# Kernel tuning notes

Measured on AMD Instinct MI355X. Metric: run time of the kernel, lower is better.

## Reference

```python
import jax, jax.numpy as jnp
import numpy as np

N_NODES = 100000
N_EDGES = 3200000
N_FEAT = 128
N_GRAPHS = 512


def setup_inputs() -> dict:
    key = jax.random.key(0)
    ks = jax.random.split(key, 12)
    x = jax.random.normal(ks[0], (N_NODES, N_FEAT), dtype=jnp.float32)
    edge_index = jax.random.randint(ks[1], (2, N_EDGES), 0, N_NODES, dtype=jnp.int64)
    batch = jnp.sort(jax.random.randint(ks[2], (N_NODES,), 0, N_GRAPHS, dtype=jnp.int64))
    def glorot(k, shape):
        lim = float(np.sqrt(6.0 / (shape[0] + shape[1])))
        return jax.random.uniform(k, shape, jnp.float32, -lim, lim)
    return {
        "x": x,
        "edge_index": edge_index,
        "batch": batch,
        "W1": glorot(ks[3], (N_FEAT, 32)),
        "b1": jnp.zeros((32,), jnp.float32),
        "W2": glorot(ks[4], (32, 64)),
        "b2": jnp.zeros((64,), jnp.float32),
        "fW1": glorot(ks[5], (96, 128)),
        "fb1": jnp.zeros((128,), jnp.float32),
        "fW2": glorot(ks[6], (128, 1)),
        "fb2": jnp.zeros((1,), jnp.float32),
    }


def _gcn_conv(h, W, b, src, dst, norm, n):
    # linear transform then normalized scatter-add aggregation (PyG GCNConv)
    h = h @ W                               # [N, out]
    msg = h[src] * norm[:, None]            # gather + scale, [E+N, out]
    agg = jax.ops.segment_sum(msg, dst, num_segments=n)
    return agg + b


def reference(x, edge_index, batch, W1, b1, W2, b2, fW1, fb1, fW2, fb2):
    n = x.shape[0]
    loop = jnp.arange(n, dtype=edge_index.dtype)
    src = jnp.concatenate([edge_index[0], loop])  # add self-loops
    dst = jnp.concatenate([edge_index[1], loop])
    # symmetric normalization: D^{-1/2} A_hat D^{-1/2}
    deg = jax.ops.segment_sum(jnp.ones(src.shape, x.dtype), dst, num_segments=n)
    dinv = jnp.where(deg > 0, jax.lax.rsqrt(deg), 0.0)
    norm = dinv[src] * dinv[dst]

    x1 = jax.nn.relu(_gcn_conv(x, W1, b1, src, dst, norm, n))   # [N, 32]
    x2 = jax.nn.relu(_gcn_conv(x1, W2, b2, src, dst, norm, n))  # [N, 64]
    xj = jnp.concatenate([x1, x2], axis=-1)                      # JK 'cat' -> [N, 96]

    # global_mean_pool over graphs
    sums = jax.ops.segment_sum(xj, batch, num_segments=N_GRAPHS)
    cnt = jax.ops.segment_sum(jnp.ones((n,), x.dtype), batch, num_segments=N_GRAPHS)
    pooled = sums / jnp.maximum(cnt, 1.0)[:, None]               # [G, 96]

    h = jax.nn.relu(pooled @ fW1 + fb1)
    return (h @ fW2 + fb2).reshape(-1)                           # [G]
```

## Files before the change

kernel.cpp:

```cpp
#include <hip/hip_runtime.h>
#include <stdint.h>

#define FEAT_IN 128
#define F1 32
#define F2 64
#define FJ 96
#define FH 128

#define BSH 8
#define BNODES 256
#define NBMAX 512
#define CH 4096
#define SRCBITS 17
#define SRCMASK 0x1FFFFu
#define PADMAX 768
#define PNPB 256
#define NP2 64
#define GR 64
#define XPAD 132

__device__ __forceinline__ unsigned f2bf(float f) {
    unsigned u = __float_as_uint(f);
    return (u + 0x7FFFu + ((u >> 16) & 1u)) >> 16;
}
__device__ __forceinline__ float bf2f(unsigned h) { return __uint_as_float(h << 16); }
__device__ __forceinline__ void bfacc8(float* a, uint4 v) {
    a[0] += bf2f(v.x & 0xffffu); a[1] += bf2f(v.x >> 16);
    a[2] += bf2f(v.y & 0xffffu); a[3] += bf2f(v.y >> 16);
    a[4] += bf2f(v.z & 0xffffu); a[5] += bf2f(v.z >> 16);
    a[6] += bf2f(v.w & 0xffffu); a[7] += bf2f(v.w >> 16);
}
__device__ __forceinline__ void fma4(float* acc, float s, float4 wv) {
    acc[0] = fmaf(s, wv.x, acc[0]);
    acc[1] = fmaf(s, wv.y, acc[1]);
    acc[2] = fmaf(s, wv.z, acc[2]);
    acc[3] = fmaf(s, wv.w, acc[3]);
}

__global__ void histPB(const int* __restrict__ dst, int* __restrict__ gHistT,
                       int nE, int nB, int nChP) {
    __shared__ int h[NBMAX];
    int ck = blockIdx.x, t = threadIdx.x;
    int e0 = ck * CH;
    int ecnt = min(CH, nE - e0);
    if (ecnt <= 0) return;
    for (int i = t; i < nB; i += 256) h[i] = 0;
    __syncthreads();
    for (int i = t; i < ecnt; i += 256) atomicAdd(&h[dst[e0 + i] >> BSH], 1);
    __syncthreads();
    for (int b = t; b < nB; b += 256) gHistT[(size_t)b * nChP + ck] = h[b];
}

__global__ void __launch_bounds__(256)
scanWB(const int* __restrict__ gHistT, int* __restrict__ gBaseT,
       int* __restrict__ btot, int nB, int nChP) {
    int wv = blockIdx.x * 4 + (threadIdx.x >> 6);
    if (wv >= nB) return;
    int lane = threadIdx.x & 63;
    const int* hp = gHistT + (size_t)wv * nChP;
    int* gp = gBaseT + (size_t)wv * nChP;
    int running = 0;
    for (int c0 = 0; c0 < nChP; c0 += 64) {
        int ck = c0 + lane;
        int v = (ck < nChP) ? hp[ck] : 0;
        int incl = v;
#pragma unroll
        for (int off = 1; off < 64; off <<= 1) {
            int u = __shfl_up(incl, off);
            if (lane >= off) incl += u;
        }
        if (ck < nChP) gp[ck] = running + incl - v;
        running += __shfl(incl, 63);
    }
    if (lane == 0) btot[wv] = running;
}

__global__ void __launch_bounds__(512)
scanOff(const int* __restrict__ btot, int* __restrict__ boff, int nB) {
    __shared__ int ps[512];
    int t = threadIdx.x;
    int v = (t < nB) ? btot[t] : 0;
    ps[t] = v; __syncthreads();
    for (int off = 1; off < 512; off <<= 1) {
        int u = (t >= off) ? ps[t - off] : 0; __syncthreads();
        ps[t] += u; __syncthreads();
    }
    int excl = ps[t] - v;
    if (t < nB) boff[t] = excl;
    if (t == nB - 1) boff[nB] = excl + v;
}

__global__ void __launch_bounds__(256)
scatterEB2(const int* __restrict__ src, const int* __restrict__ dst,
           const int* __restrict__ gBaseT, const int* __restrict__ boff,
           unsigned* __restrict__ EB, int nE, int nB, int nChP) {
    __shared__ int lh[NBMAX], loff[NBMAX], lcur[NBMAX], gbaseL[NBMAX];
    __shared__ int ps[256];
    __shared__ unsigned stagePack[CH];
    __shared__ unsigned short stageBkt[CH];
    int ck = blockIdx.x, t = threadIdx.x;
    int e0 = ck * CH;
    int ecnt = min(CH, nE - e0);
    if (ecnt <= 0) return;
    for (int i = t; i < nB; i += 256) lh[i] = 0;
    __syncthreads();
    for (int i = t; i < ecnt; i += 256) atomicAdd(&lh[dst[e0 + i] >> BSH], 1);
    __syncthreads();
    int b0 = 2 * t, b1 = 2 * t + 1;
    int c0 = (b0 < nB) ? lh[b0] : 0;
    int c1 = (b1 < nB) ? lh[b1] : 0;
    ps[t] = c0 + c1; __syncthreads();
    for (int off = 1; off < 256; off <<= 1) {
        int v = (t >= off) ? ps[t - off] : 0; __syncthreads();
        ps[t] += v; __syncthreads();
    }
    int excl = ps[t] - (c0 + c1);
    if (b0 < nB) { loff[b0] = excl;      lcur[b0] = excl;      gbaseL[b0] = boff[b0] + gBaseT[(size_t)b0 * nChP + ck]; }
    if (b1 < nB) { loff[b1] = excl + c0; lcur[b1] = excl + c0; gbaseL[b1] = boff[b1] + gBaseT[(size_t)b1 * nChP + ck]; }
    __syncthreads();
    for (int i = t; i < ecnt; i += 256) {
        int d = dst[e0 + i], s = src[e0 + i];
        int bkt = d >> BSH;
        int p = atomicAdd(&lcur[bkt], 1);
        stagePack[p] = (unsigned)s | ((unsigned)(d & (BNODES - 1)) << SRCBITS);
        stageBkt[p] = (unsigned short)bkt;
    }
    __syncthreads();
    for (int i = t; i < ecnt; i += 256) {
        int bb = stageBkt[i];
        EB[gbaseL[bb] + (i - loff[bb])] = stagePack[i];
    }
}

__global__ void __launch_bounds__(512)
bucketSortK(const unsigned* __restrict__ EB, const int* __restrict__ boff,
            int* __restrict__ rowptr, int* __restrict__ rowend, int* __restrict__ csrP,
            float* __restrict__ dinv, float* __restrict__ rs, int nN, int nB) {
    __shared__ int hist[BNODES];
    __shared__ int cur[BNODES];
    __shared__ int ps[256];
    int b = blockIdx.x, t = threadIdx.x;
    int beg = boff[b], end = boff[b + 1];
    if (t < 256) hist[t] = 0;
    __syncthreads();
    for (int i = beg + t; i < end; i += 512) atomicAdd(&hist[EB[i] >> SRCBITS], 1);
    __syncthreads();
    int deg = (t < 256) ? hist[t] : 0;
    int pdeg = (deg + 3) & ~3;
    if (t < 256) ps[t] = pdeg;
    __syncthreads();
    for (int off = 1; off < 256; off <<= 1) {
        int v = (t >= off && t < 256) ? ps[t - off] : 0; __syncthreads();
        if (t < 256) ps[t] += v;
        __syncthreads();
    }
    int base = ((beg + 3) & ~3) + b * PADMAX;
    int excl = 0;
    if (t < 256) {
        excl = base + ps[t] - pdeg;
        int node = (b << BSH) + t;
        if (node < nN) {
            rowptr[node] = excl;
            rowend[node] = excl + pdeg;
            dinv[node] = rsqrtf((float)deg + 1.0f);
            rs[node] = sqrtf((float)deg + 1.0f);
        }
        cur[t] = excl;
    }
    __syncthreads();
    for (int i = beg + t; i < end; i += 512) {
        unsigned v = EB[i];
        int p = atomicAdd(&cur[v >> SRCBITS], 1);
        csrP[p] = (int)(v & SRCMASK);
    }
    __syncthreads();
    if (t < 256) {
        for (int p = cur[t]; p < excl + pdeg; ++p) csrP[p] = nN;
    }
}

__global__ void __launch_bounds__(256)
gemm1v3(const float4* __restrict__ x4, const float* __restrict__ W1,
        const float* __restrict__ dinv, unsigned* __restrict__ Gc, int nN) {
    __shared__ float Ws[FEAT_IN * F1];
    __shared__ float xs[GR * XPAD];
    int t = threadIdx.x;
    for (int i = t; i < FEAT_IN * F1; i += 256) Ws[i] = W1[i];
    int rb = blockIdx.x * GR;
    for (int i = t; i < GR * 32; i += 256) {
        int r = i >> 5, c = i & 31;
        int row = rb + r;
        float4 v = (row < nN) ? x4[(size_t)row * 32 + c] : make_float4(0.f, 0.f, 0.f, 0.f);
        *(float4*)(xs + r * XPAD + c * 4) = v;
    }
    __syncthreads();
    int cg = t & 7, rg = t >> 3;
    int r0 = rg * 2, r1 = r0 + 1;
    int j0 = cg * 4;
    float acc0[4] = {0.f, 0.f, 0.f, 0.f};
    float acc1[4] = {0.f, 0.f, 0.f, 0.f};
    const float4* xa4 = (const float4*)(xs + r0 * XPAD);
    const float4* xb4 = (const float4*)(xs + r1 * XPAD);
    const float4* W4 = (const float4*)Ws;
#pragma unroll 4
    for (int kc = 0; kc < 32; ++kc) {
        float4 xa = xa4[kc];
        float4 xb = xb4[kc];
        float4 w0 = W4[(4 * kc + 0) * 8 + cg];
        float4 w1 = W4[(4 * kc + 1) * 8 + cg];
        float4 w2 = W4[(4 * kc + 2) * 8 + cg];
        float4 w3 = W4[(4 * kc + 3) * 8 + cg];
        fma4(acc0, xa.x, w0); fma4(acc0, xa.y, w1);
        fma4(acc0, xa.z, w2); fma4(acc0, xa.w, w3);
        fma4(acc1, xb.x, w0); fma4(acc1, xb.y, w1);
        fma4(acc1, xb.z, w2); fma4(acc1, xb.w, w3);
    }
    int c = j0 >> 4;
    int w = (j0 & 15) >> 1;
    int row0 = rb + r0, row1 = rb + r1;
    if (row0 < nN) {
        float dv = dinv[row0];
        uint2 val;
        val.x = f2bf(acc0[0] * dv) | (f2bf(acc0[1] * dv) << 16);
        val.y = f2bf(acc0[2] * dv) | (f2bf(acc0[3] * dv) << 16);
        *(uint2*)(Gc + ((size_t)c * (nN + 1) + row0) * 8 + w) = val;
    }
    if (row1 < nN) {
        float dv = dinv[row1];
        uint2 val;
        val.x = f2bf(acc1[0] * dv) | (f2bf(acc1[1] * dv) << 16);
        val.y = f2bf(acc1[2] * dv) | (f2bf(acc1[3] * dv) << 16);
        *(uint2*)(Gc + ((size_t)c * (nN + 1) + row1) * 8 + w) = val;
    }
}

__global__ void __launch_bounds__(256)
agg1v2(const int* __restrict__ rowptr, const int* __restrict__ rowend,
       const int* __restrict__ csrP, const unsigned* __restrict__ Gc,
       const float* __restrict__ dinv, const float* __restrict__ b1,
       unsigned* __restrict__ Hc, int nN, int K) {
    int b = blockIdx.x;
    int xcd = b & 7;
    int c = xcd & 1;
    int k = (b >> 3) * 4 + (xcd >> 1);
    if (k >= K) return;
    int t = threadIdx.x, wv = t >> 6, lane = t & 63;
    int node = k * 16 + wv * 4 + (lane >> 4);
    int slot = (lane >> 1) & 7, comp = lane & 1;
    bool vn = node < nN;
    const uint4* Gch = (const uint4*)(Gc + (size_t)c * (nN + 1) * 8);
    float a[8] = {0, 0, 0, 0, 0, 0, 0, 0};
    if (vn) {
        if ((lane & 14) == 0) bfacc8(a, Gch[(size_t)node * 2 + comp]);
        int beg = rowptr[node], endp = rowend[node];
        for (int e = beg + slot * 4; e < endp; e += 32) {
            int4 idx = *(const int4*)(csrP + e);
            uint4 r0 = Gch[(size_t)idx.x * 2 + comp];
            uint4 r1 = Gch[(size_t)idx.y * 2 + comp];
            uint4 r2 = Gch[(size_t)idx.z * 2 + comp];
            uint4 r3 = Gch[(size_t)idx.w * 2 + comp];
            bfacc8(a, r0); bfacc8(a, r1); bfacc8(a, r2); bfacc8(a, r3);
        }
    }
#pragma unroll
    for (int m = 2; m < 16; m <<= 1) {
#pragma unroll
        for (int i = 0; i < 8; ++i) a[i] += __shfl_xor(a[i], m);
    }
    if (vn && (lane & 14) == 0) {
        float dv = dinv[node];
        const float* bb = b1 + c * 16 + comp * 8;
        float h[8];
#pragma unroll
        for (int i = 0; i < 8; ++i) {
            float x1 = fmaxf(fmaf(dv, a[i], bb[i]), 0.f);
            h[i] = dv * x1;
        }
        uint4 hp;
        hp.x = f2bf(h[0]) | (f2bf(h[1]) << 16);
        hp.y = f2bf(h[2]) | (f2bf(h[3]) << 16);
        hp.z = f2bf(h[4]) | (f2bf(h[5]) << 16);
        hp.w = f2bf(h[6]) | (f2bf(h[7]) << 16);
        ((uint4*)(Hc + (size_t)c * (nN + 1) * 8))[(size_t)node * 2 + comp] = hp;
    }
}

__global__ void __launch_bounds__(256)
agg2v2(const int* __restrict__ rowptr, const int* __restrict__ rowend,
       const int* __restrict__ csrP, const unsigned* __restrict__ Hc,
       const float* __restrict__ dinv, float* __restrict__ A2, int nN, int K) {
    int b = blockIdx.x;
    int xcd = b & 7;
    int c = xcd & 1;
    int k = (b >> 3) * 4 + (xcd >> 1);
    if (k >= K) return;
    int t = threadIdx.x, wv = t >> 6, lane = t & 63;
    int node = k * 16 + wv * 4 + (lane >> 4);
    int slot = (lane >> 1) & 7, comp = lane & 1;
    bool vn = node < nN;
    const uint4* Hch = (const uint4*)(Hc + (size_t)c * (nN + 1) * 8);
    float a[8] = {0, 0, 0, 0, 0, 0, 0, 0};
    if (vn) {
        if ((lane & 14) == 0) bfacc8(a, Hch[(size_t)node * 2 + comp]);
        int beg = rowptr[node], endp = rowend[node];
        for (int e = beg + slot * 4; e < endp; e += 32) {
            int4 idx = *(const int4*)(csrP + e);
            uint4 r0 = Hch[(size_t)idx.x * 2 + comp];
            uint4 r1 = Hch[(size_t)idx.y * 2 + comp];
            uint4 r2 = Hch[(size_t)idx.z * 2 + comp];
            uint4 r3 = Hch[(size_t)idx.w * 2 + comp];
            bfacc8(a, r0); bfacc8(a, r1); bfacc8(a, r2); bfacc8(a, r3);
        }
    }
#pragma unroll
    for (int m = 2; m < 16; m <<= 1) {
#pragma unroll
        for (int i = 0; i < 8; ++i) a[i] += __shfl_xor(a[i], m);
    }
    if (vn && (lane & 14) == 0) {
        float dv = dinv[node];
        float* dst = A2 + (size_t)node * F1 + c * 16 + comp * 8;
        float4 o0 = make_float4(dv * a[0], dv * a[1], dv * a[2], dv * a[3]);
        float4 o1 = make_float4(dv * a[4], dv * a[5], dv * a[6], dv * a[7]);
        ((float4*)dst)[0] = o0;
        ((float4*)dst)[1] = o1;
    }
}

__global__ void __launch_bounds__(256)
poolX1(const unsigned* __restrict__ Hc, const float* __restrict__ rs,
       const int* __restrict__ batch, float* __restrict__ psum, int nN) {
    int t = threadIdx.x, wv = t >> 6, lane = t & 63;
    int c = wv >> 1, half = wv & 1;
    int base = blockIdx.x * PNPB + half * (PNPB / 2);
    int w32 = lane & 7, noff = lane >> 3;
    const unsigned* Hch = Hc + (size_t)c * (nN + 1) * 8;
    int feat = c * 16 + w32 * 2;
    float a0 = 0.f, a1 = 0.f;
    int curG = -1;
#pragma unroll 4
    for (int i = 0; i < PNPB / 16; ++i) {
        int node = base + noff + 8 * i;
        if (node >= nN) break;
        int bg = batch[node];
        if (bg != curG) {
            if (curG >= 0) {
                atomicAdd(&psum[(size_t)curG * FJ + feat + 0], a0);
                atomicAdd(&psum[(size_t)curG * FJ + feat + 1], a1);
            }
            a0 = a1 = 0.f; curG = bg;
        }
        unsigned v = Hch[(size_t)node * 8 + w32];
        float r = rs[node];
        a0 = fmaf(bf2f(v & 0xffffu), r, a0);
        a1 = fmaf(bf2f(v >> 16), r, a1);
    }
    if (curG >= 0) {
        atomicAdd(&psum[(size_t)curG * FJ + feat + 0], a0);
        atomicAdd(&psum[(size_t)curG * FJ + feat + 1], a1);
    }
}

__global__ void __launch_bounds__(256)
poolX2(const float* __restrict__ A2, const float* __restrict__ W2,
       const float* __restrict__ b2, const int* __restrict__ batch,
       float* __restrict__ psum, int nN) {
    __shared__ float W2s[F1 * F2];
    __shared__ float aL[NP2][F1];
    int t = threadIdx.x;
    for (int i = t; i < F1 * F2; i += 256) W2s[i] = W2[i];
    int nbase = blockIdx.x * NP2;
    {
        const float4* A4 = (const float4*)(A2 + (size_t)nbase * F1);
        float4* aL4 = (float4*)aL;
        int total4 = NP2 * F1 / 4;
        for (int i = t; i < total4; i += 256) {
            int gnode = nbase + (i >> 3);
            aL4[i] = (gnode < nN) ? A4[i] : make_float4(0.f, 0.f, 0.f, 0.f);
        }
    }
    __syncthreads();
    int wv = t >> 6, lane = t & 63;
    int n0 = wv * (NP2 / 4);
    float bj = b2[lane];
    float acc = 0.f;
    int curG = -1;
    for (int i = 0; i < NP2 / 4; ++i) {
        int node = nbase + n0 + i;
        if (node >= nN) break;
        int bg = batch[node];
        if (bg != curG) {
            if (curG >= 0) atomicAdd(&psum[(size_t)curG * FJ + F1 + lane], acc);
            acc = 0.f; curG = bg;
        }
        const float* a = aL[n0 + i];
        float dot = 0.f;
#pragma unroll
        for (int k = 0; k < F1; ++k) dot = fmaf(a[k], W2s[k * F2 + lane], dot);
        acc += fmaxf(dot + bj, 0.f);
    }
    if (curG >= 0) atomicAdd(&psum[(size_t)curG * FJ + F1 + lane], acc);
}

__global__ void cntBS(const int* __restrict__ batch, float* __restrict__ cnt,
                      int nN, int nG) {
    int g = blockIdx.x * blockDim.x + threadIdx.x;
    if (g >= nG) return;
    int lo = 0, hi = nN;
    while (lo < hi) { int m = (lo + hi) >> 1; if (batch[m] < g) lo = m + 1; else hi = m; }
    int s = lo;
    lo = 0; hi = nN;
    while (lo < hi) { int m = (lo + hi) >> 1; if (batch[m] < g + 1) lo = m + 1; else hi = m; }
    cnt[g] = (float)(lo - s);
}

__global__ void mlp_kernel(const float* __restrict__ psum, const float* __restrict__ cnt,
                           const float* __restrict__ fW1, const float* __restrict__ fb1,
                           const float* __restrict__ fW2, const float* __restrict__ fb2,
                           float* __restrict__ out) {
    __shared__ float p[FJ];
    __shared__ float red[FH];
    int g = blockIdx.x, tid = threadIdx.x;
    float c = fmaxf(cnt[g], 1.0f);
    if (tid < FJ) p[tid] = psum[g * FJ + tid] / c;
    __syncthreads();
    float acc = fb1[tid];
    for (int k = 0; k < FJ; ++k) acc = fmaf(p[k], fW1[k * FH + tid], acc);
    float h = fmaxf(acc, 0.f);
    red[tid] = h * fW2[tid];
    __syncthreads();
    for (int s = FH / 2; s > 0; s >>= 1) {
        if (tid < s) red[tid] += red[tid + s];
        __syncthreads();
    }
    if (tid == 0) out[g] = red[0] + fb2[0];
}

extern "C" void kernel_launch(void* const* d_in, const int* in_sizes, int n_in,
                              void* d_out, int out_size, void* d_ws, size_t ws_size,
                              hipStream_t stream) {
    const float* x   = (const float*)d_in[0];
    const int*   ei  = (const int*)d_in[1];
    const int*   bat = (const int*)d_in[2];
    const float* W1  = (const float*)d_in[3];
    const float* b1  = (const float*)d_in[4];
    const float* W2  = (const float*)d_in[5];
    const float* b2  = (const float*)d_in[6];
    const float* fW1 = (const float*)d_in[7];
    const float* fb1 = (const float*)d_in[8];
    const float* fW2 = (const float*)d_in[9];
    const float* fb2 = (const float*)d_in[10];
    float* out = (float*)d_out;

    int nN = in_sizes[0] / FEAT_IN;
    int nE = in_sizes[1] / 2;
    int nG = out_size;
    const int* src = ei;
    const int* dst = ei + nE;

    int nB   = (nN + BNODES - 1) >> BSH;
    int nCh  = (nE + CH - 1) / CH;
    int nChP = (nCh + 3) & ~3;
    int K    = (nN + 15) / 16;
    int gridC = ((K + 3) / 4) * 8;

    char* w = (char*)d_ws;
    auto alloc = [&](size_t bytes) { char* p = w; w += (bytes + 15) & ~(size_t)15; return p; };
    int*      gHistT = (int*)alloc((size_t)NBMAX * nChP * 4);
    int*      gBaseT = (int*)alloc((size_t)NBMAX * nChP * 4);
    int*      btot   = (int*)alloc(NBMAX * 4);
    int*      boff   = (int*)alloc((NBMAX + 1) * 4);
    unsigned* EB     = (unsigned*)alloc((size_t)nE * 4);
    int*      rowptr = (int*)alloc((size_t)nN * 4);
    int*      rowend = (int*)alloc((size_t)nN * 4);
    int*      csrP   = (int*)alloc(((size_t)nE + (size_t)NBMAX * PADMAX + 64) * 4);
    float*    dinv   = (float*)alloc((size_t)nN * 4);
    float*    rsb    = (float*)alloc((size_t)nN * 4);
    unsigned* Gc     = (unsigned*)alloc((size_t)2 * (nN + 1) * 16 * 2);
    unsigned* Hc     = (unsigned*)alloc((size_t)2 * (nN + 1) * 16 * 2);
    float*    A2     = (float*)alloc((size_t)(nN + NP2) * F1 * 4);
    float*    psum   = (float*)alloc((size_t)nG * FJ * 4);
    float*    cnt    = (float*)alloc((size_t)nG * 4);

    hipMemsetAsync(gHistT, 0, (size_t)nB * nChP * 4, stream);
    hipMemsetAsync(psum, 0, (size_t)nG * FJ * 4, stream);
    for (int c = 0; c < 2; ++c) {
        hipMemsetAsync(Gc + ((size_t)c * (nN + 1) + nN) * 16, 0, 32, stream);
        hipMemsetAsync(Hc + ((size_t)c * (nN + 1) + nN) * 16, 0, 32, stream);
    }

    histPB<<<nCh, 256, 0, stream>>>(dst, gHistT, nE, nB, nChP);
    scanWB<<<(nB + 3) / 4, 256, 0, stream>>>(gHistT, gBaseT, btot, nB, nChP);
    scanOff<<<1, 512, 0, stream>>>(btot, boff, nB);
    scatterEB2<<<nCh, 256, 0, stream>>>(src, dst, gBaseT, boff, EB, nE, nB, nChP);
    bucketSortK<<<nB, 512, 0, stream>>>(EB, boff, rowptr, rowend, csrP, dinv, rsb, nN, nB);

    gemm1v3<<<(nN + GR - 1) / GR, 256, 0, stream>>>((const float4*)x, W1, dinv, Gc, nN);
    agg1v2<<<gridC, 256, 0, stream>>>(rowptr, rowend, csrP, Gc, dinv, b1, Hc, nN, K);
    agg2v2<<<gridC, 256, 0, stream>>>(rowptr, rowend, csrP, Hc, dinv, A2, nN, K);

    poolX1<<<(nN + PNPB - 1) / PNPB, 256, 0, stream>>>(Hc, rsb, bat, psum, nN);
    poolX2<<<(nN + NP2 - 1) / NP2, 256, 0, stream>>>(A2, W2, b2, bat, psum, nN);
    cntBS<<<(nG + 255) / 256, 256, 0, stream>>>(bat, cnt, nN, nG);
    mlp_kernel<<<nG, FH, 0, stream>>>(psum, cnt, fW1, fb1, fW2, fb2, out);
}
```

Before: 254.3 us.

## Store layer-2 aggregate in bf16, fold memsets and count kernel into others

Several independent tweaks. The layer-2 aggregate A2 is now written as packed bf16 instead of fp32, halving that intermediate's traffic, and poolX2 unpacks it into shared memory. The four small pad-row memsets are replaced by writes inside gemm1v3, and the separate cntBS kernel is folded into mlp_kernel via a per-block binary search. The histogram layout becomes chunk-major, so histPB writes contiguously while scanWB reads strided, and bf16 unpacking of the high half uses a mask instead of a shift. The bf16 storage adds rounding error to the layer-2 input before the W2 transform.

```diff
diff --git a/kernel.cpp b/kernel.cpp
--- a/kernel.cpp
+++ b/kernel.cpp
@@ -23,12 +23,13 @@
     unsigned u = __float_as_uint(f);
     return (u + 0x7FFFu + ((u >> 16) & 1u)) >> 16;
 }
-__device__ __forceinline__ float bf2f(unsigned h) { return __uint_as_float(h << 16); }
+__device__ __forceinline__ float bf2f_lo(unsigned u) { return __uint_as_float(u << 16); }
+__device__ __forceinline__ float bf2f_hi(unsigned u) { return __uint_as_float(u & 0xffff0000u); }
 __device__ __forceinline__ void bfacc8(float* a, uint4 v) {
-    a[0] += bf2f(v.x & 0xffffu); a[1] += bf2f(v.x >> 16);
-    a[2] += bf2f(v.y & 0xffffu); a[3] += bf2f(v.y >> 16);
-    a[4] += bf2f(v.z & 0xffffu); a[5] += bf2f(v.z >> 16);
-    a[6] += bf2f(v.w & 0xffffu); a[7] += bf2f(v.w >> 16);
+    a[0] += bf2f_lo(v.x); a[1] += bf2f_hi(v.x);
+    a[2] += bf2f_lo(v.y); a[3] += bf2f_hi(v.y);
+    a[4] += bf2f_lo(v.z); a[5] += bf2f_hi(v.z);
+    a[6] += bf2f_lo(v.w); a[7] += bf2f_hi(v.w);
 }
 __device__ __forceinline__ void fma4(float* acc, float s, float4 wv) {
     acc[0] = fmaf(s, wv.x, acc[0]);
@@ -37,8 +38,8 @@
     acc[3] = fmaf(s, wv.w, acc[3]);
 }
 
-__global__ void histPB(const int* __restrict__ dst, int* __restrict__ gHistT,
-                       int nE, int nB, int nChP) {
+__global__ void histPB(const int* __restrict__ dst, int* __restrict__ gHist,
+                       int nE, int nB) {
     __shared__ int h[NBMAX];
     int ck = blockIdx.x, t = threadIdx.x;
     int e0 = ck * CH;
@@ -48,21 +49,20 @@
     __syncthreads();
     for (int i = t; i < ecnt; i += 256) atomicAdd(&h[dst[e0 + i] >> BSH], 1);
     __syncthreads();
-    for (int b = t; b < nB; b += 256) gHistT[(size_t)b * nChP + ck] = h[b];
-}
-
-__global__ void __launch_bounds__(256)
-scanWB(const int* __restrict__ gHistT, int* __restrict__ gBaseT,
+    for (int b = t; b < nB; b += 256) gHist[(size_t)ck * NBMAX + b] = h[b];
+}
+
+__global__ void __launch_bounds__(256)
+scanWB(const int* __restrict__ gHist, int* __restrict__ gBaseT,
        int* __restrict__ btot, int nB, int nChP) {
     int wv = blockIdx.x * 4 + (threadIdx.x >> 6);
     if (wv >= nB) return;
     int lane = threadIdx.x & 63;
-    const int* hp = gHistT + (size_t)wv * nChP;
     int* gp = gBaseT + (size_t)wv * nChP;
     int running = 0;
     for (int c0 = 0; c0 < nChP; c0 += 64) {
         int ck = c0 + lane;
-        int v = (ck < nChP) ? hp[ck] : 0;
+        int v = (ck < nChP) ? gHist[(size_t)ck * NBMAX + wv] : 0;
         int incl = v;
 #pragma unroll
         for (int off = 1; off < 64; off <<= 1) {
@@ -181,10 +181,15 @@
 
 __global__ void __launch_bounds__(256)
 gemm1v3(const float4* __restrict__ x4, const float* __restrict__ W1,
-        const float* __restrict__ dinv, unsigned* __restrict__ Gc, int nN) {
+        const float* __restrict__ dinv, unsigned* __restrict__ Gc,
+        unsigned* __restrict__ Hc, int nN) {
     __shared__ float Ws[FEAT_IN * F1];
     __shared__ float xs[GR * XPAD];
     int t = threadIdx.x;
+    if (blockIdx.x == 0 && t < 16) {
+        Gc[((size_t)(t >> 3) * (nN + 1) + nN) * 8 + (t & 7)] = 0u;
+        Hc[((size_t)(t >> 3) * (nN + 1) + nN) * 8 + (t & 7)] = 0u;
+    }
     for (int i = t; i < FEAT_IN * F1; i += 256) Ws[i] = W1[i];
     int rb = blockIdx.x * GR;
     for (int i = t; i < GR * 32; i += 256) {
@@ -288,7 +293,7 @@
 __global__ void __launch_bounds__(256)
 agg2v2(const int* __restrict__ rowptr, const int* __restrict__ rowend,
        const int* __restrict__ csrP, const unsigned* __restrict__ Hc,
-       const float* __restrict__ dinv, float* __restrict__ A2, int nN, int K) {
+       const float* __restrict__ dinv, unsigned* __restrict__ A2b, int nN, int K) {
     int b = blockIdx.x;
     int xcd = b & 7;
     int c = xcd & 1;
@@ -319,11 +324,12 @@
     }
     if (vn && (lane & 14) == 0) {
         float dv = dinv[node];
-        float* dst = A2 + (size_t)node * F1 + c * 16 + comp * 8;
-        float4 o0 = make_float4(dv * a[0], dv * a[1], dv * a[2], dv * a[3]);
-        float4 o1 = make_float4(dv * a[4], dv * a[5], dv * a[6], dv * a[7]);
-        ((float4*)dst)[0] = o0;
-        ((float4*)dst)[1] = o1;
+        uint4 o;
+        o.x = f2bf(dv * a[0]) | (f2bf(dv * a[1]) << 16);
+        o.y = f2bf(dv * a[2]) | (f2bf(dv * a[3]) << 16);
+        o.z = f2bf(dv * a[4]) | (f2bf(dv * a[5]) << 16);
+        o.w = f2bf(dv * a[6]) | (f2bf(dv * a[7]) << 16);
+        ((uint4*)(A2b + (size_t)node * 16))[c * 2 + comp] = o;
     }
 }
 
@@ -352,8 +358,8 @@
         }
         unsigned v = Hch[(size_t)node * 8 + w32];
         float r = rs[node];
-        a0 = fmaf(bf2f(v & 0xffffu), r, a0);
-        a1 = fmaf(bf2f(v >> 16), r, a1);
+        a0 = fmaf(bf2f_lo(v), r, a0);
+        a1 = fmaf(bf2f_hi(v), r, a1);
     }
     if (curG >= 0) {
         atomicAdd(&psum[(size_t)curG * FJ + feat + 0], a0);
@@ -362,7 +368,7 @@
 }
 
 __global__ void __launch_bounds__(256)
-poolX2(const float* __restrict__ A2, const float* __restrict__ W2,
+poolX2(const unsigned* __restrict__ A2b, const float* __restrict__ W2,
        const float* __restrict__ b2, const int* __restrict__ batch,
        float* __restrict__ psum, int nN) {
     __shared__ float W2s[F1 * F2];
@@ -371,12 +377,15 @@
     for (int i = t; i < F1 * F2; i += 256) W2s[i] = W2[i];
     int nbase = blockIdx.x * NP2;
     {
-        const float4* A4 = (const float4*)(A2 + (size_t)nbase * F1);
-        float4* aL4 = (float4*)aL;
-        int total4 = NP2 * F1 / 4;
-        for (int i = t; i < total4; i += 256) {
-            int gnode = nbase + (i >> 3);
-            aL4[i] = (gnode < nN) ? A4[i] : make_float4(0.f, 0.f, 0.f, 0.f);
+        const uint4* A4 = (const uint4*)(A2b + (size_t)nbase * 16);
+        for (int i = t; i < NP2 * 4; i += 256) {
+            int gnode = nbase + (i >> 2);
+            uint4 v = (gnode < nN) ? A4[i] : make_uint4(0u, 0u, 0u, 0u);
+            float* d = aL[i >> 2] + (i & 3) * 8;
+            d[0] = bf2f_lo(v.x); d[1] = bf2f_hi(v.x);
+            d[2] = bf2f_lo(v.y); d[3] = bf2f_hi(v.y);
+            d[4] = bf2f_lo(v.z); d[5] = bf2f_hi(v.z);
+            d[6] = bf2f_lo(v.w); d[7] = bf2f_hi(v.w);
         }
     }
     __syncthreads();
@@ -402,27 +411,25 @@
     if (curG >= 0) atomicAdd(&psum[(size_t)curG * FJ + F1 + lane], acc);
 }
 
-__global__ void cntBS(const int* __restrict__ batch, float* __restrict__ cnt,
-                      int nN, int nG) {
-    int g = blockIdx.x * blockDim.x + threadIdx.x;
-    if (g >= nG) return;
-    int lo = 0, hi = nN;
-    while (lo < hi) { int m = (lo + hi) >> 1; if (batch[m] < g) lo = m + 1; else hi = m; }
-    int s = lo;
-    lo = 0; hi = nN;
-    while (lo < hi) { int m = (lo + hi) >> 1; if (batch[m] < g + 1) lo = m + 1; else hi = m; }
-    cnt[g] = (float)(lo - s);
-}
-
-__global__ void mlp_kernel(const float* __restrict__ psum, const float* __restrict__ cnt,
+__global__ void mlp_kernel(const float* __restrict__ psum, const int* __restrict__ batch,
+                           int nN,
                            const float* __restrict__ fW1, const float* __restrict__ fb1,
                            const float* __restrict__ fW2, const float* __restrict__ fb2,
                            float* __restrict__ out) {
     __shared__ float p[FJ];
     __shared__ float red[FH];
+    __shared__ float cinv;
     int g = blockIdx.x, tid = threadIdx.x;
-    float c = fmaxf(cnt[g], 1.0f);
-    if (tid < FJ) p[tid] = psum[g * FJ + tid] / c;
+    if (tid == 0) {
+        int lo = 0, hi = nN;
+        while (lo < hi) { int m = (lo + hi) >> 1; if (batch[m] < g) lo = m + 1; else hi = m; }
+        int s = lo;
+        lo = 0; hi = nN;
+        while (lo < hi) { int m = (lo + hi) >> 1; if (batch[m] < g + 1) lo = m + 1; else hi = m; }
+        cinv = 1.0f / fmaxf((float)(lo - s), 1.0f);
+    }
+    __syncthreads();
+    if (tid < FJ) p[tid] = psum[g * FJ + tid] * cinv;
     __syncthreads();
     float acc = fb1[tid];
     for (int k = 0; k < FJ; ++k) acc = fmaf(p[k], fW1[k * FH + tid], acc);
@@ -466,7 +473,7 @@
 
     char* w = (char*)d_ws;
     auto alloc = [&](size_t bytes) { char* p = w; w += (bytes + 15) & ~(size_t)15; return p; };
-    int*      gHistT = (int*)alloc((size_t)NBMAX * nChP * 4);
+    int*      gHist  = (int*)alloc((size_t)nChP * NBMAX * 4);
     int*      gBaseT = (int*)alloc((size_t)NBMAX * nChP * 4);
     int*      btot   = (int*)alloc(NBMAX * 4);
     int*      boff   = (int*)alloc((NBMAX + 1) * 4);
@@ -478,29 +485,23 @@
     float*    rsb    = (float*)alloc((size_t)nN * 4);
     unsigned* Gc     = (unsigned*)alloc((size_t)2 * (nN + 1) * 16 * 2);
     unsigned* Hc     = (unsigned*)alloc((size_t)2 * (nN + 1) * 16 * 2);
-    float*    A2     = (float*)alloc((size_t)(nN + NP2) * F1 * 4);
+    unsigned* A2b    = (unsigned*)alloc((size_t)(nN + NP2) * 16 * 4);
     float*    psum   = (float*)alloc((size_t)nG * FJ * 4);
-    float*    cnt    = (float*)alloc((size_t)nG * 4);
-
-    hipMemsetAsync(gHistT, 0, (size_t)nB * nChP * 4, stream);
+
+    hipMemsetAsync(gHist, 0, (size_t)nChP * NBMAX * 4, stream);
     hipMemsetAsync(psum, 0, (size_t)nG * FJ * 4, stream);
-    for (int c = 0; c < 2; ++c) {
-        hipMemsetAsync(Gc + ((size_t)c * (nN + 1) + nN) * 16, 0, 32, stream);
-        hipMemsetAsync(Hc + ((size_t)c * (nN + 1) + nN) * 16, 0, 32, stream);
-    }
-
-    histPB<<<nCh, 256, 0, stream>>>(dst, gHistT, nE, nB, nChP);
-    scanWB<<<(nB + 3) / 4, 256, 0, stream>>>(gHistT, gBaseT, btot, nB, nChP);
+
+    histPB<<<nCh, 256, 0, stream>>>(dst, gHist, nE, nB);
+    scanWB<<<(nB + 3) / 4, 256, 0, stream>>>(gHist, gBaseT, btot, nB, nChP);
     scanOff<<<1, 512, 0, stream>>>(btot, boff, nB);
     scatterEB2<<<nCh, 256, 0, stream>>>(src, dst, gBaseT, boff, EB, nE, nB, nChP);
     bucketSortK<<<nB, 512, 0, stream>>>(EB, boff, rowptr, rowend, csrP, dinv, rsb, nN, nB);
 
-    gemm1v3<<<(nN + GR - 1) / GR, 256, 0, stream>>>((const float4*)x, W1, dinv, Gc, nN);
+    gemm1v3<<<(nN + GR - 1) / GR, 256, 0, stream>>>((const float4*)x, W1, dinv, Gc, Hc, nN);
     agg1v2<<<gridC, 256, 0, stream>>>(rowptr, rowend, csrP, Gc, dinv, b1, Hc, nN, K);
-    agg2v2<<<gridC, 256, 0, stream>>>(rowptr, rowend, csrP, Hc, dinv, A2, nN, K);
+    agg2v2<<<gridC, 256, 0, stream>>>(rowptr, rowend, csrP, Hc, dinv, A2b, nN, K);
 
     poolX1<<<(nN + PNPB - 1) / PNPB, 256, 0, stream>>>(Hc, rsb, bat, psum, nN);
-    poolX2<<<(nN + NP2 - 1) / NP2, 256, 0, stream>>>(A2, W2, b2, bat, psum, nN);
-    cntBS<<<(nG + 255) / 256, 256, 0, stream>>>(bat, cnt, nN, nG);
-    mlp_kernel<<<nG, FH, 0, stream>>>(psum, cnt, fW1, fb1, fW2, fb2, out);
-}
+    poolX2<<<(nN + NP2 - 1) / NP2, 256, 0, stream>>>(A2b, W2, b2, bat, psum, nN);
+    mlp_kernel<<<nG, FH, 0, stream>>>(psum, bat, nN, fW1, fb1, fW2, fb2, out);
+}
```

After: 237.6 us. 1.07x faster.
